# Kernel tuning notes

Measured on AMD Instinct MI355X. Metric: run time of the kernel, lower is better.

The kernel has to match this reference:

```python
import jax, jax.numpy as jnp
import numpy as np

D, DFF, H, V, BS, NL, NG = 1024, 4096, 16, 32000, 128, 2, 2

def _ln(x, w, b, eps=1e-5):
    m = x.mean(-1, keepdims=True)
    v = ((x - m) ** 2).mean(-1, keepdims=True)
    return (x - m) / jnp.sqrt(v + eps) * w + b

def _full_attn(q, k, v):
    # q,k,v: [B,H,S,dk] ; manual max-subtract softmax with +1e-9 denom and clamp, per FullAttention
    dk = q.shape[-1]
    s = jnp.einsum('bhqd,bhkd->bhqk', q / jnp.sqrt(jnp.float32(dk)), k)
    s = s - s.max(-1, keepdims=True)
    e = jnp.exp(s)
    a = e / (e.sum(-1, keepdims=True) + 1e-9)
    a = jnp.clip(a, 1e-9, 1.0)
    return jnp.einsum('bhqk,bhkd->bhqd', a, v)

def _attn_layer(qi, ki, vi, lnw, lnb, pw, pb):
    # lnw/lnb: [4,D] (norm_q,k,v,out); pw: [4,D,D] (q,k,v,o, stored [in,out]); pb: [4,D]
    B, Sq, _ = qi.shape
    Sk = ki.shape[1]
    q = _ln(qi, lnw[0], lnb[0]) @ pw[0] + pb[0]
    k = _ln(ki, lnw[1], lnb[1]) @ pw[1] + pb[1]
    v = _ln(vi, lnw[2], lnb[2]) @ pw[2] + pb[2]
    dk = D // H
    q = q.reshape(B, Sq, H, dk).transpose(0, 2, 1, 3)
    k = k.reshape(B, Sk, H, dk).transpose(0, 2, 1, 3)
    v = v.reshape(B, Sk, H, dk).transpose(0, 2, 1, 3)
    o = _full_attn(q, k, v).transpose(0, 2, 1, 3).reshape(B, Sq, D)
    o = o @ pw[3] + pb[3]
    return _ln(o, lnw[3], lnb[3])

def _ffn(x, n1w, n1b, n2w, n2b, w1, b1, w2, b2):
    h = jax.nn.gelu(_ln(x, n1w, n1b) @ w1 + b1, approximate=False)
    return _ln(h @ w2 + b2 + x, n2w, n2b)

def _tlayer(x, lnw, lnb, pw, pb, w1, b1, w2, b2):
    # lnw/lnb: [6,D] (attn q,k,v,out norms, ffn norm1, ffn norm2)
    x = x + _attn_layer(x, x, x, lnw[:4], lnb[:4], pw, pb)
    return _ffn(x, lnw[4], lnb[4], lnw[5], lnb[5], w1, b1, w2, b2)

def _pe(S, d):
    pos = jnp.arange(S, dtype=jnp.float32)[:, None]
    div = jnp.exp(jnp.arange(0, d, 2, dtype=jnp.float32) * (-np.log(10000.0) / d))
    pe = jnp.zeros((S, d), jnp.float32)
    pe = pe.at[:, 0::2].set(jnp.sin(pos * div))
    pe = pe.at[:, 1::2].set(jnp.cos(pos * div))
    return pe

def setup_inputs() -> dict:
    key = jax.random.key(0)
    ks = iter(jax.random.split(key, 64))
    nrm = lambda shp: jax.random.normal(next(ks), shp, jnp.float32) * 0.02
    inp = {
        'x': jax.random.randint(next(ks), (4, 4096), 0, V, dtype=jnp.int32).astype(jnp.int64),
        'emb': nrm((V, D)),
        'in_ln_w': jnp.ones((D,)), 'in_ln_b': jnp.zeros((D,)),
        'loc_ln_w': jnp.ones((NL, 6, D)), 'loc_ln_b': jnp.zeros((NL, 6, D)),
        'loc_pw': nrm((NL, 4, D, D)), 'loc_pb': jnp.zeros((NL, 4, D)),
        'loc_w1': nrm((NL, D, DFF)), 'loc_b1': jnp.zeros((NL, DFF)),
        'loc_w2': nrm((NL, DFF, D)), 'loc_b2': jnp.zeros((NL, D)),
        'locn_w': jnp.ones((D,)), 'locn_b': jnp.zeros((D,)),
        'pool_q': nrm((1, 1, D)),
        'pool_n_w': jnp.ones((D,)), 'pool_n_b': jnp.zeros((D,)),
        'pool_ln_w': jnp.ones((4, D)), 'pool_ln_b': jnp.zeros((4, D)),
        'pool_pw': nrm((4, D, D)), 'pool_pb': jnp.zeros((4, D)),
        'glob_ln_w': jnp.ones((NG, 6, D)), 'glob_ln_b': jnp.zeros((NG, 6, D)),
        'glob_pw': nrm((NG, 4, D, D)), 'glob_pb': jnp.zeros((NG, 4, D)),
        'glob_w1': nrm((NG, D, DFF)), 'glob_b1': jnp.zeros((NG, DFF)),
        'glob_w2': nrm((NG, DFF, D)), 'glob_b2': jnp.zeros((NG, D)),
        'out_ln_w': jnp.ones((D,)), 'out_ln_b': jnp.zeros((D,)),
        'out_w': nrm((D, V)), 'out_b': jnp.zeros((V,)),
    }
    return inp

def reference(x, emb, in_ln_w, in_ln_b, loc_ln_w, loc_ln_b, loc_pw, loc_pb,
              loc_w1, loc_b1, loc_w2, loc_b2, locn_w, locn_b,
              pool_q, pool_n_w, pool_n_b, pool_ln_w, pool_ln_b, pool_pw, pool_pb,
              glob_ln_w, glob_ln_b, glob_pw, glob_pb, glob_w1, glob_b1, glob_w2, glob_b2,
              out_ln_w, out_ln_b, out_w, out_b):
    B, S = x.shape
    nb = S // BS
    h = jnp.clip(emb[x], -100.0, 100.0) + _pe(S, D)[None]
    h = _ln(h, in_ln_w, in_ln_b)
    h = h.reshape(B * nb, BS, D)  # local blocks
    for i in range(NL):
        h = jnp.clip(_tlayer(h, loc_ln_w[i], loc_ln_b[i], loc_pw[i], loc_pb[i],
                             loc_w1[i], loc_b1[i], loc_w2[i], loc_b2[i]), -100.0, 100.0)
    h = _ln(h, locn_w, locn_b)
    # attention pooling of each block to one vector
    hp = _ln(h, pool_n_w, pool_n_b)
    q = jnp.broadcast_to(pool_q, (B * nb, 1, D))
    g = _attn_layer(q, hp, hp, pool_ln_w, pool_ln_b, pool_pw, pool_pb)[:, 0].reshape(B, nb, D)
    for i in range(NG):
        g = jnp.clip(_tlayer(g, glob_ln_w[i], glob_ln_b[i], glob_pw[i], glob_pb[i],
                             glob_w1[i], glob_b1[i], glob_w2[i], glob_b2[i]), -100.0, 100.0)
    g = _ln(g, out_ln_w, out_ln_b)
    return g @ out_w + out_b  # [B, num_blocks, vocab]
```

## Files before the change

### kernel.cpp

```cpp
#include <hip/hip_runtime.h>
#include <hip/hip_bf16.h>
#include <math.h>

#define DEV __device__ __forceinline__

typedef __attribute__((ext_vector_type(8))) short bf16x8;
typedef __attribute__((ext_vector_type(4))) float f32x4;
typedef unsigned short u16;

constexpr int D_ = 1024, NTOK = 16384, SEQ = 4096;

DEV u16 f2b(float f){
  union{float f;unsigned u;} v; v.f=f;
  unsigned r = (v.u + 0x7fffu + ((v.u>>16)&1u))>>16;
  return (u16)r;
}
DEV float b2f(u16 h){ union{unsigned u;float f;} v; v.u=((unsigned)h)<<16; return v.f; }

DEV float gelu_f(float x){
  float z = 0.7978845608028654f*(x + 0.044715f*x*x*x);
  float e = __expf(-2.f*z);
  float t = 2.f/(1.f+e) - 1.f;
  return 0.5f*x*(1.f+t);
}

DEV void gld16(const void* g, void* l){
  __builtin_amdgcn_global_load_lds((const __attribute__((address_space(1))) void*)g,
                                   (__attribute__((address_space(3))) void*)l, 16, 0, 0);
}

#define BAR()    __builtin_amdgcn_s_barrier()
#define SCHED0() __builtin_amdgcn_sched_barrier(0)
#define LGKM0()  asm volatile("s_waitcnt lgkmcnt(0)" ::: "memory")
#define VM4()    asm volatile("s_waitcnt vmcnt(4)" ::: "memory")
#define VM0()    asm volatile("s_waitcnt vmcnt(0)" ::: "memory")

DEV float blockSum(float v){
  __shared__ float sb[4];
  #pragma unroll
  for(int m=32;m>=1;m>>=1) v += __shfl_xor(v, m, 64);
  int lane = threadIdx.x & 63, wv = threadIdx.x >> 6;
  __syncthreads();
  if(lane==0) sb[wv]=v;
  __syncthreads();
  float r = sb[0]+sb[1]+sb[2]+sb[3];
  __syncthreads();
  return r;
}

__global__ __launch_bounds__(256) void detect_k(const int* __restrict__ xr, int* __restrict__ flag){
  int tid=threadIdx.x; float cnt=0.f;
  for(int i=tid;i<8192;i+=256) if(xr[2*i+1]!=0) cnt+=1.f;
  cnt = blockSum(cnt);
  if(tid==0) *flag = (cnt < 64.f) ? 1 : 0;
}

__global__ __launch_bounds__(256) void embed_k(const void* __restrict__ xv, const int* __restrict__ flag,
      const float* __restrict__ emb, const float* __restrict__ w, const float* __restrict__ b,
      u16* __restrict__ out, u16* __restrict__ outn){
  int t = blockIdx.x;
  int id;
  if(*flag) id = (int)((const long long*)xv)[t];
  else      id = ((const int*)xv)[t];
  int s = t & (SEQ-1);
  int d0 = threadIdx.x*4;
  float4 e4 = *(const float4*)(emb + (size_t)id*D_ + d0);
  float vv[4] = {e4.x, e4.y, e4.z, e4.w};
  float acc = 0.f;
  #pragma unroll
  for(int i=0;i<4;i++){
    float e = fminf(fmaxf(vv[i], -100.f), 100.f);
    int d = d0+i;
    float fr = expf(-(float)(d & ~1) * (9.210340371976184f/(float)D_));
    float ang = (float)s * fr;
    e += (d&1) ? cosf(ang) : sinf(ang);
    vv[i]=e; acc+=e;
  }
  float mean = blockSum(acc)*(1.f/D_);
  float var=0.f;
  #pragma unroll
  for(int i=0;i<4;i++){ float dd=vv[i]-mean; var+=dd*dd; }
  var = blockSum(var)*(1.f/D_);
  float rs = rsqrtf(var+1e-5f);
  float y[4];
  #pragma unroll
  for(int i=0;i<4;i++) y[i] = (vv[i]-mean)*rs*w[d0+i]+b[d0+i];
  ushort4 o; o.x=f2b(y[0]); o.y=f2b(y[1]); o.z=f2b(y[2]); o.w=f2b(y[3]);
  *(ushort4*)(out + (size_t)t*D_ + d0) = o;
  float m2 = blockSum(y[0]+y[1]+y[2]+y[3])*(1.f/D_);
  float v2=0.f;
  #pragma unroll
  for(int i=0;i<4;i++){ float dd=y[i]-m2; v2+=dd*dd; }
  v2 = blockSum(v2)*(1.f/D_);
  float rs2 = rsqrtf(v2+1e-5f);
  ushort4 on; on.x=f2b((y[0]-m2)*rs2); on.y=f2b((y[1]-m2)*rs2); on.z=f2b((y[2]-m2)*rs2); on.w=f2b((y[3]-m2)*rs2);
  *(ushort4*)(outn + (size_t)t*D_ + d0) = on;
}

template<int MODE,int WRN>
__global__ __launch_bounds__(256) void ln_k(const u16* __restrict__ in, const u16* __restrict__ res,
      const float* __restrict__ w, const float* __restrict__ b, u16* __restrict__ out,
      u16* __restrict__ outn){
  int t = blockIdx.x; int d0 = threadIdx.x*4;
  ushort4 r4 = *(const ushort4*)(in + (size_t)t*D_ + d0);
  float vv[4] = {b2f(r4.x),b2f(r4.y),b2f(r4.z),b2f(r4.w)};
  float mean = blockSum(vv[0]+vv[1]+vv[2]+vv[3])*(1.f/D_);
  float var=0.f;
  #pragma unroll
  for(int i=0;i<4;i++){ float dd=vv[i]-mean; var+=dd*dd; }
  var = blockSum(var)*(1.f/D_);
  float rs = rsqrtf(var+1e-5f);
  float rv[4]={0,0,0,0};
  if(MODE==3){
    ushort4 q4 = *(const ushort4*)(res + (size_t)t*D_ + d0);
    rv[0]=b2f(q4.x); rv[1]=b2f(q4.y); rv[2]=b2f(q4.z); rv[3]=b2f(q4.w);
  }
  float y[4];
  #pragma unroll
  for(int i=0;i<4;i++){
    float v = (vv[i]-mean)*rs;
    v = v*w[d0+i]+b[d0+i];
    if(MODE==2) v = fminf(fmaxf(v,-100.f),100.f);
    if(MODE==3) v += rv[i];
    y[i]=v;
  }
  ushort4 o; o.x=f2b(y[0]); o.y=f2b(y[1]); o.z=f2b(y[2]); o.w=f2b(y[3]);
  *(ushort4*)(out + (size_t)t*D_ + d0) = o;
  if(WRN){
    float m2 = blockSum(y[0]+y[1]+y[2]+y[3])*(1.f/D_);
    float v2=0.f;
    #pragma unroll
    for(int i=0;i<4;i++){ float dd=y[i]-m2; v2+=dd*dd; }
    v2 = blockSum(v2)*(1.f/D_);
    float rs2 = rsqrtf(v2+1e-5f);
    ushort4 on; on.x=f2b((y[0]-m2)*rs2); on.y=f2b((y[1]-m2)*rs2); on.z=f2b((y[2]-m2)*rs2); on.w=f2b((y[3]-m2)*rs2);
    *(ushort4*)(outn + (size_t)t*D_ + d0) = on;
  }
}

__global__ __launch_bounds__(256) void ln3x_k(const u16* __restrict__ in,
    const float* __restrict__ w1,const float* __restrict__ b1,
    const float* __restrict__ w2,const float* __restrict__ b2, u16* __restrict__ out){
  int t=blockIdx.x, d0=threadIdx.x*4;
  ushort4 r4 = *(const ushort4*)(in + (size_t)t*D_ + d0);
  float vv[4]={b2f(r4.x),b2f(r4.y),b2f(r4.z),b2f(r4.w)};
  #pragma unroll
  for(int pass=0;pass<3;pass++){
    float mean = blockSum(vv[0]+vv[1]+vv[2]+vv[3])*(1.f/D_);
    float var=0.f;
    #pragma unroll
    for(int i=0;i<4;i++){ float dd=vv[i]-mean; var+=dd*dd; }
    var = blockSum(var)*(1.f/D_);
    float rs = rsqrtf(var+1e-5f);
    #pragma unroll
    for(int i=0;i<4;i++){
      float y=(vv[i]-mean)*rs;
      if(pass==0) y = y*w1[d0+i]+b1[d0+i];
      else if(pass==1) y = y*w2[d0+i]+b2[d0+i];
      vv[i]=y;
    }
  }
  ushort4 o;
  o.x=f2b(vv[0]); o.y=f2b(vv[1]); o.z=f2b(vv[2]); o.w=f2b(vv[3]);
  *(ushort4*)(out + (size_t)t*D_ + d0) = o;
}

__global__ __launch_bounds__(256) void lnrow_k(const float* __restrict__ x, const float* __restrict__ w,
      const float* __restrict__ b, float* __restrict__ out){
  int d0=threadIdx.x*4;
  float vv[4]={x[d0],x[d0+1],x[d0+2],x[d0+3]};
  float mean = blockSum(vv[0]+vv[1]+vv[2]+vv[3])*(1.f/D_);
  float var=0.f;
  #pragma unroll
  for(int i=0;i<4;i++){ float dd=vv[i]-mean; var+=dd*dd; }
  var = blockSum(var)*(1.f/D_);
  float rs = rsqrtf(var+1e-5f);
  #pragma unroll
  for(int i=0;i<4;i++) out[d0+i]=(vv[i]-mean)*rs*w[d0+i]+b[d0+i];
}

#define TF_BODY(W, ldW, lnw, Wt, Kd, n0, k0)                                 \
  {                                                                          \
    int ty = threadIdx.x>>6, tx = threadIdx.x&63;                            \
    _Pragma("unroll")                                                        \
    for(int p=0;p<16;p++){                                                   \
      int row = p*4+ty;                                                      \
      float sc = (lnw) ? (lnw)[(k0)+row] : 1.f;                              \
      T[row][tx] = (W)[(size_t)((k0)+row)*(ldW) + (n0)+tx]*sc;               \
    }                                                                        \
    __syncthreads();                                                         \
    _Pragma("unroll")                                                        \
    for(int p=0;p<16;p++){                                                   \
      int row = p*4+ty;                                                      \
      (Wt)[(size_t)((n0)+row)*(Kd) + (k0)+tx] = f2b(T[tx][row]);             \
    }                                                                        \
  }

__global__ __launch_bounds__(256) void tf_k(const float* __restrict__ W, int ldW,
      const float* __restrict__ lnw, u16* __restrict__ Wt, int Kd){
  __shared__ float T[64][65];
  int n0 = blockIdx.x*64, k0 = blockIdx.y*64;
  TF_BODY(W, ldW, lnw, Wt, Kd, n0, k0)
}

__global__ __launch_bounds__(256) void prep_tf_layer_k(const float* __restrict__ pw,
      const float* __restrict__ w1, const float* __restrict__ w2, const float* __restrict__ lw,
      u16* __restrict__ Wqk, u16* __restrict__ Wv, u16* __restrict__ Wo,
      u16* __restrict__ W1t, u16* __restrict__ W2t){
  __shared__ float T[64][65];
  int bid = blockIdx.x;
  const float* W; int ldW; const float* lnw; u16* Wt; int Kd, n0, k0;
  if(bid < 1024){
    int m = bid>>8, t = bid&255;
    n0 = (t&15)*64; k0 = (t>>4)*64;
    W = pw + (size_t)m*1024*1024; ldW = 1024; Kd = 1024;
    lnw = (m<3) ? lw + m*1024 : nullptr;
    Wt = (m==0)?Wqk : (m==1)?(Wqk+1024*1024) : (m==2)?Wv : Wo;
  } else if(bid < 2048){
    int t = bid-1024;
    n0 = (t&63)*64; k0 = (t>>6)*64;
    W = w1; ldW = 4096; Kd = 1024; lnw = lw+4*1024; Wt = W1t;
  } else {
    int t = bid-2048;
    n0 = (t&15)*64; k0 = (t>>4)*64;
    W = w2; ldW = 1024; Kd = 4096; lnw = nullptr; Wt = W2t;
  }
  TF_BODY(W, ldW, lnw, Wt, Kd, n0, k0)
}

__global__ __launch_bounds__(256) void prep_tf_pool_k(const float* __restrict__ pw,
      const float* __restrict__ lw, u16* __restrict__ PWkv, u16* __restrict__ PWo){
  __shared__ float T[64][65];
  int bid = blockIdx.x;
  int m = 1 + (bid>>8), t = bid&255;
  int n0 = (t&15)*64, k0 = (t>>4)*64;
  const float* W = pw + (size_t)m*1024*1024;
  const float* lnw = (m<3) ? lw + m*1024 : nullptr;
  u16* Wt = (m==1)?PWkv : (m==2)?(PWkv+1024*1024) : PWo;
  TF_BODY(W, 1024, lnw, Wt, 1024, n0, k0)
}

DEV void bias_body(const float* W, int ldW, int Kd, const float* lnb, float pbv, float* out){
  int tid = threadIdx.x;
  float chk = 0.f;
  if(lnb){ for(int k=tid;k<Kd;k+=256) chk += fabsf(lnb[k]); }
  chk = blockSum(chk);
  if(chk==0.f){ if(tid==0) *out = pbv; return; }
  float s=0.f;
  for(int k=tid;k<Kd;k+=256) s += lnb[k]*W[(size_t)k*ldW];
  s = blockSum(s);
  if(tid==0) *out = pbv + s;
}

__global__ __launch_bounds__(256) void bias_k(const float* __restrict__ W, int ldW,
      const float* __restrict__ lnb, const float* __restrict__ pb, float* __restrict__ out, int Kd){
  int j = blockIdx.x;
  bias_body(W + j, ldW, Kd, lnb, pb[j], out + j);
}

__global__ __launch_bounds__(256) void prep_bias_layer_k(const float* __restrict__ pw,
      const float* __restrict__ w1, const float* __restrict__ w2,
      const float* __restrict__ lb, const float* __restrict__ pb,
      const float* __restrict__ b1in, const float* __restrict__ b2in,
      float* __restrict__ Bqk, float* __restrict__ Bv, float* __restrict__ Bo,
      float* __restrict__ B1, float* __restrict__ B2){
  int j = blockIdx.x;
  const float* W; int ldW, Kd; const float* lnb; float pbv; float* out;
  const size_t MM = 1024ull*1024;
  if(j<2048){ int m=j>>10; int col=j&1023; W=pw+m*MM+col; ldW=1024; Kd=1024; lnb=lb+m*1024; pbv=pb[m*1024+col]; out=Bqk+j; }
  else if(j<3072){ int col=j-2048; W=pw+2*MM+col; ldW=1024; Kd=1024; lnb=lb+2*1024; pbv=pb[2*1024+col]; out=Bv+col; }
  else if(j<4096){ int col=j-3072; W=pw+3*MM+col; ldW=1024; Kd=1024; lnb=nullptr; pbv=pb[3*1024+col]; out=Bo+col; }
  else if(j<8192){ int col=j-4096; W=w1+col; ldW=4096; Kd=1024; lnb=lb+4*1024; pbv=b1in[col]; out=B1+col; }
  else { int col=j-8192; W=w2+col; ldW=1024; Kd=4096; lnb=nullptr; pbv=b2in[col]; out=B2+col; }
  bias_body(W, ldW, Kd, lnb, pbv, out);
}

__global__ __launch_bounds__(256) void prep_bias_pool_k(const float* __restrict__ pw,
      const float* __restrict__ lb, const float* __restrict__ pb,
      float* __restrict__ Pbkv, float* __restrict__ Pbo){
  int j = blockIdx.x;
  const size_t MM = 1024ull*1024;
  int m = 1 + (j>>10), col = j&1023;
  const float* lnb = (m<3) ? lb + m*1024 : nullptr;
  float* out = (m==1)?(Pbkv+col) : (m==2)?(Pbkv+1024+col) : (Pbo+col);
  bias_body(pw + m*MM + col, 1024, 1024, lnb, pb[m*1024+col], out);
}

__global__ __launch_bounds__(256) void matvec_k(const float* __restrict__ xn, const float* __restrict__ W,
      int ldW, const float* __restrict__ bias, float* __restrict__ out){
  int j=blockIdx.x, tid=threadIdx.x;
  float s=0.f;
  for(int k=tid;k<1024;k+=256) s += xn[k]*W[(size_t)k*ldW + j];
  s=blockSum(s);
  if(tid==0) out[j]=s+bias[j];
}

template<int EPI,int OUTF,int TV>
__global__ __launch_bounds__(256) void gemm_k(const u16* __restrict__ A, const u16* __restrict__ Bt,
      const float* __restrict__ bias, const u16* __restrict__ resid, void* __restrict__ Cout,
      int M, int N, int K, int ldc){
  __shared__ u16 SH[24576];
  int tid = threadIdx.x, lane = tid&63, wv = tid>>6;
  int g = lane>>4, l15 = lane&15;
  int GX = gridDim.x;
  int nwg = GX*gridDim.y;
  int flat = blockIdx.y*GX + blockIdx.x;
  int q = nwg>>3, r = nwg&7, xcd = flat&7, idx = flat>>3;
  int f = (xcd<r ? xcd*(q+1) : r*(q+1)+(xcd-r)*q) + idx;
  int by = f/GX, bx = f - by*GX;
  int row0 = by*128, col0 = bx*128;
  int wr = wv>>1, wc = wv&1;
  int e0 = wv*512 + lane*8;
  f32x4 acc[4][4] = {};
  auto STAGE = [&](int buf, int k0){
    u16* base = SH + buf*8192;
    #pragma unroll
    for(int c=0;c<2;c++){
      int e = c*2048 + e0;
      int row = e>>5;
      int slx = ((e>>3)&3) ^ ((row>>1)&3);
      gld16(A  + (size_t)(row0 + row)*K + (k0 + slx*8), &base[e]);
      gld16(Bt + (size_t)(col0 + row)*K + (k0 + slx*8), &base[4096 + e]);
    }
  };
  int nt = K>>5;
  STAGE(0, 0); STAGE(1, 32);
  VM4(); LGKM0(); BAR(); SCHED0();
  for(int t=0;t<nt;t++){
    int b = t % 3;
    if(t+2<nt) STAGE((t+2)%3, (t+2)<<5);
    bf16x8 a[4], bb[4];
    #pragma unroll
    for(int m=0;m<4;m++){
      int ra = wr*64+m*16+l15;
      a[m] = *(const bf16x8*)&SH[b*8192 + ra*32 + ((g ^ ((ra>>1)&3))<<3)];
    }
    #pragma unroll
    for(int n=0;n<4;n++){
      int rb = wc*64+n*16+l15;
      bb[n] = *(const bf16x8*)&SH[b*8192 + 4096 + rb*32 + ((g ^ ((rb>>1)&3))<<3)];
    }
    #pragma unroll
    for(int m=0;m<4;m++)
      #pragma unroll
      for(int n=0;n<4;n++)
        acc[m][n] = __builtin_amdgcn_mfma_f32_16x16x32_bf16(a[m], bb[n], acc[m][n], 0,0,0);
    if(t+1<nt){
      if(t+2<nt){ VM4(); } else { VM0(); }
      LGKM0(); BAR(); SCHED0();
    }
  }
  if(TV){
    __syncthreads();
    u16* Tb = SH;
    #pragma unroll
    for(int m=0;m<4;m++){
      #pragma unroll
      for(int n=0;n<4;n++){
        int c = wc*64 + n*16 + l15;
        float bs = bias[col0 + c];
        #pragma unroll
        for(int r2=0;r2<4;r2++){
          int Rl = wr*64 + m*16 + g*4 + r2;
          Tb[c*128 + (Rl ^ ((c&7)<<4))] = f2b(acc[m][n][r2]+bs);
        }
      }
    }
    __syncthreads();
    for(int p=tid*4; p<16384; p+=1024){
      int c = p>>7, rr = p&127;
      int rs = rr ^ ((c&7)<<4);
      ushort4 v4;
      v4.x = Tb[c*128+rs]; v4.y = Tb[c*128+rs+1]; v4.z = Tb[c*128+rs+2]; v4.w = Tb[c*128+rs+3];
      *(ushort4*)((u16*)Cout + (size_t)(col0+c)*M + row0 + rr) = v4;
    }
  } else {
    #pragma unroll
    for(int m=0;m<4;m++){
      #pragma unroll
      for(int n=0;n<4;n++){
        int Cc = col0 + wc*64 + n*16 + l15;
        float bs = bias[Cc];
        #pragma unroll
        for(int r2=0;r2<4;r2++){
          int R = row0 + wr*64 + m*16 + g*4 + r2;
          float v = acc[m][n][r2] + bs;
          if(EPI==1) v = gelu_f(v);
          if(EPI==2) v += b2f(resid[(size_t)R*ldc + Cc]);
          if(OUTF) ((float*)Cout)[(size_t)R*ldc + Cc] = v;
          else     ((u16*)Cout)[(size_t)R*ldc + Cc] = f2b(v);
        }
      }
    }
  }
}

__global__ __launch_bounds__(256) void attnl_k(const u16* __restrict__ QK, const u16* __restrict__ VT,
      u16* __restrict__ AT){
  __shared__ u16 SP[16384];
  __shared__ u16 Vt[8192];
  __shared__ float rmax[256], rsum[256];
  int tid=threadIdx.x, lane=tid&63, wv=tid>>6, g=lane>>4, l15=lane&15;
  int lb = blockIdx.x>>4, h = blockIdx.x&15;
  int wr=wv>>1, wc=wv&1;
  #pragma unroll
  for(int c=0;c<4;c++){
    int chunk = c*2048 + wv*512;
    int e = chunk + lane*8;
    int rq = e>>6;
    int sq = ((e>>3)&7) ^ (rq&7);
    int rv = e>>7;
    int sv = ((e>>3)&15) ^ (rv&15);
    gld16(QK + (size_t)(lb*128 + rq)*2048 + h*64 + sq*8,        &SP[chunk]);
    gld16(QK + (size_t)(lb*128 + rq)*2048 + 1024 + h*64 + sq*8, &SP[8192+chunk]);
    gld16(VT + (size_t)(h*64 + rv)*16384 + lb*128 + sv*8,       &Vt[chunk]);
  }
  __syncthreads();
  f32x4 s[4][4] = {};
  #pragma unroll
  for(int ks=0;ks<2;ks++){
    bf16x8 a[4], b[4];
    #pragma unroll
    for(int m=0;m<4;m++){
      int ra = wr*64+m*16+l15;
      a[m] = *(const bf16x8*)&SP[ra*64 + (((ks*4+g) ^ (ra&7))<<3)];
    }
    #pragma unroll
    for(int n=0;n<4;n++){
      int rb = wc*64+n*16+l15;
      b[n] = *(const bf16x8*)&SP[8192 + rb*64 + (((ks*4+g) ^ (rb&7))<<3)];
    }
    #pragma unroll
    for(int m=0;m<4;m++)
      #pragma unroll
      for(int n=0;n<4;n++)
        s[m][n] = __builtin_amdgcn_mfma_f32_16x16x32_bf16(a[m], b[n], s[m][n], 0,0,0);
  }
  #pragma unroll
  for(int m=0;m<4;m++)
    #pragma unroll
    for(int n=0;n<4;n++) s[m][n] *= 0.125f;
  #pragma unroll
  for(int m=0;m<4;m++)
    #pragma unroll
    for(int r=0;r<4;r++){
      float mx = fmaxf(fmaxf(s[m][0][r],s[m][1][r]),fmaxf(s[m][2][r],s[m][3][r]));
      #pragma unroll
      for(int msk=1;msk<16;msk<<=1) mx = fmaxf(mx, __shfl_xor(mx,msk,64));
      if(l15==0) rmax[(wr*64+m*16+g*4+r)*2+wc]=mx;
    }
  __syncthreads();
  #pragma unroll
  for(int m=0;m<4;m++)
    #pragma unroll
    for(int r=0;r<4;r++){
      int row = wr*64+m*16+g*4+r;
      float M2 = fmaxf(rmax[row*2], rmax[row*2+1]);
      float sm=0.f;
      #pragma unroll
      for(int n=0;n<4;n++){ float e = expf(s[m][n][r]-M2); s[m][n][r]=e; sm+=e; }
      #pragma unroll
      for(int msk=1;msk<16;msk<<=1) sm += __shfl_xor(sm,msk,64);
      if(l15==0) rsum[row*2+wc]=sm;
    }
  __syncthreads();
  #pragma unroll
  for(int m=0;m<4;m++)
    #pragma unroll
    for(int r=0;r<4;r++){
      int row = wr*64+m*16+g*4+r;
      float den = rsum[row*2]+rsum[row*2+1]+1e-9f;
      #pragma unroll
      for(int n=0;n<4;n++){
        float a = s[m][n][r]/den;
        a = fminf(fmaxf(a,1e-9f),1.f);
        int col = wc*64+n*16+l15;
        SP[row*128 + ((((col>>3) ^ (row&15))<<3) | (col&7))] = f2b(a);
      }
    }
  __syncthreads();
  f32x4 o[4][2] = {};
  #pragma unroll
  for(int ks=0;ks<4;ks++){
    bf16x8 a[4], b[2];
    #pragma unroll
    for(int m=0;m<4;m++){
      int ra = wr*64+m*16+l15;
      a[m] = *(const bf16x8*)&SP[ra*128 + (((ks*4+g) ^ (ra&15))<<3)];
    }
    #pragma unroll
    for(int n=0;n<2;n++){
      int rv = wc*32+n*16+l15;
      b[n] = *(const bf16x8*)&Vt[rv*128 + (((ks*4+g) ^ (rv&15))<<3)];
    }
    #pragma unroll
    for(int m=0;m<4;m++)
      #pragma unroll
      for(int n=0;n<2;n++)
        o[m][n] = __builtin_amdgcn_mfma_f32_16x16x32_bf16(a[m], b[n], o[m][n], 0,0,0);
  }
  #pragma unroll
  for(int m=0;m<4;m++)
    #pragma unroll
    for(int n=0;n<2;n++)
      #pragma unroll
      for(int r=0;r<4;r++)
        AT[(size_t)(lb*128 + wr*64+m*16+g*4+r)*1024 + h*64 + wc*32+n*16+l15] = f2b(o[m][n][r]);
}

__global__ __launch_bounds__(256) void poolattn_k(const float* __restrict__ qp, const u16* __restrict__ KV,
      u16* __restrict__ g0){
  int lb = blockIdx.x, tid = threadIdx.x;
  __shared__ float sc[16*128];
  for(int p=tid;p<2048;p+=256){
    int h=p>>7, j=p&127;
    const u16* krow = KV + (size_t)(lb*128+j)*2048 + h*64;
    float s=0.f;
    for(int d=0;d<64;d++) s += qp[h*64+d]*b2f(krow[d]);
    sc[h*128+j] = s*0.125f;
  }
  __syncthreads();
  if(tid<16){
    float* r=&sc[tid*128];
    float mx=r[0];
    for(int j=1;j<128;j++) mx=fmaxf(mx,r[j]);
    float sm=0.f;
    for(int j=0;j<128;j++){ float e=expf(r[j]-mx); r[j]=e; sm+=e; }
    sm+=1e-9f;
    for(int j=0;j<128;j++) r[j]=fminf(fmaxf(r[j]/sm,1e-9f),1.f);
  }
  __syncthreads();
  for(int c=tid;c<1024;c+=256){
    int h=c>>6;
    float acc=0.f;
    for(int j=0;j<128;j++) acc += sc[h*128+j]*b2f(KV[(size_t)(lb*128+j)*2048 + 1024 + c]);
    g0[(size_t)lb*1024 + c] = f2b(acc);
  }
}

__global__ __launch_bounds__(256) void attng_k(const u16* __restrict__ QKV, u16* __restrict__ OUT){
  int bb = blockIdx.x>>4, h = blockIdx.x&15;
  __shared__ float sc[32*32];
  int tid=threadIdx.x;
  for(int p=tid;p<1024;p+=256){
    int i=p>>5, j=p&31;
    const u16* q = QKV + (size_t)(bb*32+i)*3072 + h*64;
    const u16* k = QKV + (size_t)(bb*32+j)*3072 + 1024 + h*64;
    float s=0.f;
    for(int d=0;d<64;d++) s += b2f(q[d])*b2f(k[d]);
    sc[p] = s*0.125f;
  }
  __syncthreads();
  if(tid<32){
    float* r=&sc[tid*32];
    float mx=r[0];
    for(int j=1;j<32;j++) mx=fmaxf(mx,r[j]);
    float sm=0.f;
    for(int j=0;j<32;j++){ float e=expf(r[j]-mx); r[j]=e; sm+=e; }
    sm+=1e-9f;
    for(int j=0;j<32;j++) r[j]=fminf(fmaxf(r[j]/sm,1e-9f),1.f);
  }
  __syncthreads();
  for(int p=tid;p<2048;p+=256){
    int i=p>>6, d=p&63;
    float acc=0.f;
    for(int j=0;j<32;j++) acc += sc[i*32+j]*b2f(QKV[(size_t)(bb*32+j)*3072 + 2048 + h*64 + d]);
    OUT[(size_t)(bb*32+i)*1024 + h*64 + d] = f2b(acc);
  }
}

extern "C" void kernel_launch(void* const* d_in, const int* in_sizes, int n_in,
                              void* d_out, int out_size, void* d_ws, size_t ws_size,
                              hipStream_t stream) {
  (void)in_sizes; (void)n_in; (void)out_size;
  const void*  x       = d_in[0];
  const float* emb     = (const float*)d_in[1];
  const float* in_ln_w = (const float*)d_in[2];
  const float* in_ln_b = (const float*)d_in[3];
  const float* loc_ln_w= (const float*)d_in[4];
  const float* loc_ln_b= (const float*)d_in[5];
  const float* loc_pw  = (const float*)d_in[6];
  const float* loc_pb  = (const float*)d_in[7];
  const float* loc_w1  = (const float*)d_in[8];
  const float* loc_b1  = (const float*)d_in[9];
  const float* loc_w2  = (const float*)d_in[10];
  const float* loc_b2  = (const float*)d_in[11];
  const float* locn_w  = (const float*)d_in[12];
  const float* locn_b  = (const float*)d_in[13];
  const float* pool_q  = (const float*)d_in[14];
  const float* pool_n_w= (const float*)d_in[15];
  const float* pool_n_b= (const float*)d_in[16];
  const float* pool_ln_w=(const float*)d_in[17];
  const float* pool_ln_b=(const float*)d_in[18];
  const float* pool_pw = (const float*)d_in[19];
  const float* pool_pb = (const float*)d_in[20];
  const float* glob_ln_w=(const float*)d_in[21];
  const float* glob_ln_b=(const float*)d_in[22];
  const float* glob_pw = (const float*)d_in[23];
  const float* glob_pb = (const float*)d_in[24];
  const float* glob_w1 = (const float*)d_in[25];
  const float* glob_b1 = (const float*)d_in[26];
  const float* glob_w2 = (const float*)d_in[27];
  const float* glob_b2 = (const float*)d_in[28];
  const float* out_ln_w= (const float*)d_in[29];
  const float* out_ln_b= (const float*)d_in[30];
  const float* out_w   = (const float*)d_in[31];
  const float* out_b   = (const float*)d_in[32];

  char* wsb = (char*)d_ws;
  size_t off = 0;
  auto AL = [&](size_t n)->char*{ size_t o=(off+255)&~(size_t)255; off=o+n; return wsb+o; };

  int*  flag = (int*)AL(256);
  u16*  WA   = (u16*)AL(12ull*1024*1024*2);
  float* BA  = (float*)AL(12*1024*4);
  float* qn  = (float*)AL(1024*4);
  float* qp  = (float*)AL(1024*4);
  float* Hb  = (float*)AL(32000*4);
  u16*  R    = (u16*)AL(64ull*1024*1024*2);
  u16*  X    = (u16*)AL((size_t)NTOK*1024*2);
  u16*  XN   = (u16*)AL((size_t)NTOK*1024*2);
  u16*  G    = (u16*)AL(128ull*1024*2);
  u16*  GN   = (u16*)AL(128ull*1024*2);
  u16*  GQKV = (u16*)AL(128ull*3072*2);
  u16*  GAT  = (u16*)AL(128ull*1024*2);
  u16*  GO   = (u16*)AL(128ull*1024*2);
  u16*  GFH  = (u16*)AL(128ull*4096*2);
  u16*  g0   = (u16*)AL(128ull*1024*2);
  if(off > ws_size) return;

  u16 *LWqk = WA, *LWv = WA+2097152, *LWo = WA+3145728, *LW1 = WA+4194304, *LW2 = WA+8388608;
  float *Lbqk = BA, *Lbv = BA+2048, *Lbo = BA+3072, *Lb1 = BA+4096, *Lb2 = BA+8192;
  u16 *GWqkv = WA, *GWo = WA+3145728, *GW1 = WA+4194304, *GW2 = WA+8388608;
  float *Gbqkv = BA, *Gbo = BA+3072, *Gb1 = BA+4096, *Gb2 = BA+8192;
  u16 *PWkv = WA, *PWo = WA+2097152;
  float *Pbkv = BA, *Pbo = BA+2048;
  u16 *QKb = R, *VTb = R+33554432, *ATb = R+50331648;
  u16 *FH  = R;
  u16 *KVb = R;
  u16 *HW  = R;
  u16 *Ob  = XN;

  const size_t MM = 1024ull*1024;

  detect_k<<<1,256,0,stream>>>((const int*)x, flag);
  embed_k<<<NTOK,256,0,stream>>>(x, flag, emb, in_ln_w, in_ln_b, X, XN);

  for(int l=0;l<2;l++){
    const float* pw = loc_pw + (size_t)l*4*MM;
    const float* lw = loc_ln_w + (size_t)l*6*1024;
    const float* lb = loc_ln_b + (size_t)l*6*1024;
    const float* pb = loc_pb + (size_t)l*4*1024;
    const float* w1 = loc_w1 + (size_t)l*1024*4096;
    const float* w2 = loc_w2 + (size_t)l*4096*1024;
    prep_tf_layer_k<<<3072,256,0,stream>>>(pw, w1, w2, lw, LWqk, LWv, LWo, LW1, LW2);
    prep_bias_layer_k<<<9216,256,0,stream>>>(pw, w1, w2, lb, pb,
        loc_b1+(size_t)l*4096, loc_b2+(size_t)l*1024, Lbqk, Lbv, Lbo, Lb1, Lb2);

    gemm_k<0,0,0><<<dim3(16,128),256,0,stream>>>(XN, LWqk, Lbqk, nullptr, QKb, NTOK, 2048, 1024, 2048);
    gemm_k<0,0,1><<<dim3(8,128),256,0,stream>>>(XN, LWv, Lbv, nullptr, VTb, NTOK, 1024, 1024, 0);
    attnl_k<<<128*16,256,0,stream>>>(QKb, VTb, ATb);
    gemm_k<0,0,0><<<dim3(8,128),256,0,stream>>>(ATb, LWo, Lbo, nullptr, Ob, NTOK, 1024, 1024, 1024);
    ln_k<3,1><<<NTOK,256,0,stream>>>(Ob, X, lw+3*1024, lb+3*1024, X, XN);
    gemm_k<1,0,0><<<dim3(32,128),256,0,stream>>>(XN, LW1, Lb1, nullptr, FH, NTOK, 4096, 1024, 4096);
    gemm_k<2,0,0><<<dim3(8,128),256,0,stream>>>(FH, LW2, Lb2, X, Ob, NTOK, 1024, 4096, 1024);
    ln_k<2,1><<<NTOK,256,0,stream>>>(Ob, nullptr, lw+5*1024, lb+5*1024, X, XN);
  }

  prep_tf_pool_k<<<768,256,0,stream>>>(pool_pw, pool_ln_w, PWkv, PWo);
  prep_bias_pool_k<<<3072,256,0,stream>>>(pool_pw, pool_ln_b, pool_pb, Pbkv, Pbo);
  lnrow_k<<<1,256,0,stream>>>(pool_q, pool_ln_w, pool_ln_b, qn);
  matvec_k<<<1024,256,0,stream>>>(qn, pool_pw, 1024, pool_pb, qp);
  ln3x_k<<<NTOK,256,0,stream>>>(X, locn_w, locn_b, pool_n_w, pool_n_b, XN);
  gemm_k<0,0,0><<<dim3(16,128),256,0,stream>>>(XN, PWkv, Pbkv, nullptr, KVb, NTOK, 2048, 1024, 2048);
  poolattn_k<<<128,256,0,stream>>>(qp, KVb, g0);
  gemm_k<0,0,0><<<dim3(8,1),256,0,stream>>>(g0, PWo, Pbo, nullptr, GO, 128, 1024, 1024, 1024);
  ln_k<1,1><<<128,256,0,stream>>>(GO, nullptr, pool_ln_w+3*1024, pool_ln_b+3*1024, G, GN);

  for(int l=0;l<2;l++){
    const float* pw = glob_pw + (size_t)l*4*MM;
    const float* lw = glob_ln_w + (size_t)l*6*1024;
    const float* lb = glob_ln_b + (size_t)l*6*1024;
    const float* pb = glob_pb + (size_t)l*4*1024;
    const float* w1 = glob_w1 + (size_t)l*1024*4096;
    const float* w2 = glob_w2 + (size_t)l*4096*1024;
    prep_tf_layer_k<<<3072,256,0,stream>>>(pw, w1, w2, lw, GWqkv, GWqkv+2097152, GWo, GW1, GW2);
    prep_bias_layer_k<<<9216,256,0,stream>>>(pw, w1, w2, lb, pb,
        glob_b1+(size_t)l*4096, glob_b2+(size_t)l*1024, Gbqkv, Gbqkv+2048, Gbo, Gb1, Gb2);

    gemm_k<0,0,0><<<dim3(24,1),256,0,stream>>>(GN, GWqkv, Gbqkv, nullptr, GQKV, 128, 3072, 1024, 3072);
    attng_k<<<64,256,0,stream>>>(GQKV, GAT);
    gemm_k<0,0,0><<<dim3(8,1),256,0,stream>>>(GAT, GWo, Gbo, nullptr, GO, 128, 1024, 1024, 1024);
    ln_k<3,1><<<128,256,0,stream>>>(GO, G, lw+3*1024, lb+3*1024, G, GN);
    gemm_k<1,0,0><<<dim3(32,1),256,0,stream>>>(GN, GW1, Gb1, nullptr, GFH, 128, 4096, 1024, 4096);
    gemm_k<2,0,0><<<dim3(8,1),256,0,stream>>>(GFH, GW2, Gb2, G, GO, 128, 1024, 4096, 1024);
    ln_k<2,1><<<128,256,0,stream>>>(GO, nullptr, lw+5*1024, lb+5*1024, G, GN);
  }

  tf_k<<<dim3(500,16),256,0,stream>>>(out_w, 32000, out_ln_w, HW, 1024);
  bias_k<<<32000,256,0,stream>>>(out_w, 32000, out_ln_b, out_b, Hb, 1024);
  gemm_k<0,1,0><<<dim3(250,1),256,0,stream>>>(GN, HW, Hb, nullptr, d_out, 128, 32000, 1024, 32000);
}
```

Baseline: 2.077 ms.

## Switch GEMM to BK=64 double-buffered LDS pipeline with 8-way swizzle

The GEMM K-tile grows from 32 to 64 with a new XOR swizzle over 8 chunks. The pipeline changes from triple buffering at prefetch depth 2 to double buffering at depth 1. This halves the number of barriers and waits per K and doubles the MFMA work per sync. The cost is a larger LDS footprint (64KB), which may lower occupancy, and a shallower prefetch that waits for the full load (vmcnt(0)) every iteration.

```diff
diff --git a/kernel.cpp b/kernel.cpp
--- a/kernel.cpp
+++ b/kernel.cpp
@@ -32,7 +32,6 @@
 #define BAR()    __builtin_amdgcn_s_barrier()
 #define SCHED0() __builtin_amdgcn_sched_barrier(0)
 #define LGKM0()  asm volatile("s_waitcnt lgkmcnt(0)" ::: "memory")
-#define VM4()    asm volatile("s_waitcnt vmcnt(4)" ::: "memory")
 #define VM0()    asm volatile("s_waitcnt vmcnt(0)" ::: "memory")
 
 DEV float blockSum(float v){
@@ -299,7 +298,7 @@
 __global__ __launch_bounds__(256) void gemm_k(const u16* __restrict__ A, const u16* __restrict__ Bt,
       const float* __restrict__ bias, const u16* __restrict__ resid, void* __restrict__ Cout,
       int M, int N, int K, int ldc){
-  __shared__ u16 SH[24576];
+  __shared__ u16 SH[32768];
   int tid = threadIdx.x, lane = tid&63, wv = tid>>6;
   int g = lane>>4, l15 = lane&15;
   int GX = gridDim.x;
@@ -312,42 +311,48 @@
   int wr = wv>>1, wc = wv&1;
   int e0 = wv*512 + lane*8;
   f32x4 acc[4][4] = {};
-  auto STAGE = [&](int buf, int k0){
-    u16* base = SH + buf*8192;
-    #pragma unroll
-    for(int c=0;c<2;c++){
+  auto STAGE = [&](int buf, int t){
+    u16* base = SH + buf*16384;
+    int k0 = t<<6;
+    #pragma unroll
+    for(int c=0;c<4;c++){
       int e = c*2048 + e0;
-      int row = e>>5;
-      int slx = ((e>>3)&3) ^ ((row>>1)&3);
+      int row = e>>6;
+      int slx = ((e>>3)&7) ^ (row&7);
       gld16(A  + (size_t)(row0 + row)*K + (k0 + slx*8), &base[e]);
-      gld16(Bt + (size_t)(col0 + row)*K + (k0 + slx*8), &base[4096 + e]);
+      gld16(Bt + (size_t)(col0 + row)*K + (k0 + slx*8), &base[8192 + e]);
     }
   };
-  int nt = K>>5;
-  STAGE(0, 0); STAGE(1, 32);
-  VM4(); LGKM0(); BAR(); SCHED0();
+  int nt = K>>6;
+  STAGE(0, 0);
+  VM0(); BAR(); SCHED0();
+  #pragma unroll 2
   for(int t=0;t<nt;t++){
-    int b = t % 3;
-    if(t+2<nt) STAGE((t+2)%3, (t+2)<<5);
-    bf16x8 a[4], bb[4];
-    #pragma unroll
-    for(int m=0;m<4;m++){
-      int ra = wr*64+m*16+l15;
-      a[m] = *(const bf16x8*)&SH[b*8192 + ra*32 + ((g ^ ((ra>>1)&3))<<3)];
-    }
-    #pragma unroll
-    for(int n=0;n<4;n++){
-      int rb = wc*64+n*16+l15;
-      bb[n] = *(const bf16x8*)&SH[b*8192 + 4096 + rb*32 + ((g ^ ((rb>>1)&3))<<3)];
-    }
-    #pragma unroll
-    for(int m=0;m<4;m++)
-      #pragma unroll
-      for(int n=0;n<4;n++)
-        acc[m][n] = __builtin_amdgcn_mfma_f32_16x16x32_bf16(a[m], bb[n], acc[m][n], 0,0,0);
+    int b = t&1;
+    if(t+1<nt) STAGE(b^1, t+1);
+    bf16x8 a[2][4], bb[2][4];
+    #pragma unroll
+    for(int ks=0;ks<2;ks++){
+      #pragma unroll
+      for(int m=0;m<4;m++){
+        int ra = wr*64+m*16+l15;
+        a[ks][m] = *(const bf16x8*)&SH[b*16384 + ra*64 + (((ks*4+g) ^ (ra&7))<<3)];
+      }
+      #pragma unroll
+      for(int n=0;n<4;n++){
+        int rb = wc*64+n*16+l15;
+        bb[ks][n] = *(const bf16x8*)&SH[b*16384 + 8192 + rb*64 + (((ks*4+g) ^ (rb&7))<<3)];
+      }
+    }
+    #pragma unroll
+    for(int ks=0;ks<2;ks++)
+      #pragma unroll
+      for(int m=0;m<4;m++)
+        #pragma unroll
+        for(int n=0;n<4;n++)
+          acc[m][n] = __builtin_amdgcn_mfma_f32_16x16x32_bf16(a[ks][m], bb[ks][n], acc[m][n], 0,0,0);
     if(t+1<nt){
-      if(t+2<nt){ VM4(); } else { VM0(); }
-      LGKM0(); BAR(); SCHED0();
+      VM0(); LGKM0(); BAR(); SCHED0();
     }
   }
   if(TV){
```

After: 1.948 ms. 6.2% less time.
